# Kernel optimization log

Hardware: AMD Instinct MI355X
Metric: run time of the kernel (lower is better)

## Reference

```python
import jax, jax.numpy as jnp
import numpy as np

N = 8192
D_IN = 512
D_OUT = 64
ALPHA = 0.2  # LeakyReLU negative slope
MASK_VAL = -9e15


def setup_inputs() -> dict:
    key = jax.random.key(0)
    k1, k2, k3, k4 = jax.random.split(key, 4)
    inp = jax.random.normal(k1, (N, D_IN), dtype=jnp.float32)
    adj = (jax.random.uniform(k2, (N, N)) < 0.05).astype(jnp.float32)
    adj = adj.at[jnp.arange(N), jnp.arange(N)].set(1.0)
    W = jax.random.normal(k3, (D_IN, D_OUT), dtype=jnp.float32) * 0.05
    a = jax.random.normal(k4, (2 * D_OUT, 1), dtype=jnp.float32) * 0.05
    return {"input": inp, "adj": adj, "W": W, "a": a}


def reference(input, adj, W, a):
    # h = input @ W : [n, out]
    h = input @ W
    # Algebraic equivalent of the dense pairwise concat:
    # e_ij = leakyrelu([h_i || h_j] . a) = leakyrelu(h_i.a1 + h_j.a2)
    a1, a2 = a[:D_OUT, 0], a[D_OUT:, 0]          # [out], [out]
    e = jax.nn.leaky_relu(
        (h @ a1)[:, None] + (h @ a2)[None, :],    # [n, n]
        negative_slope=ALPHA,
    )
    attention = jnp.where(adj > 0, e, MASK_VAL)
    attention = jax.nn.softmax(attention, axis=1)
    out = attention @ h                            # [n, out]
    return jax.nn.elu(out)                         # end=False branch
```

## Files before the change

### kernel.cpp

```cpp
#include <hip/hip_runtime.h>
#include <hip/hip_bf16.h>

#define N 8192
#define D_IN 512
#define D_OUT 64
#define ALPHA 0.2f
#define BM 16
#define BK 128
#define NSH 32

typedef __attribute__((ext_vector_type(4))) float f32x4;
typedef __attribute__((ext_vector_type(8))) short bf16x8;

static __device__ __forceinline__ unsigned pk_bf16(float lo, float hi) {
    unsigned ulo = __bfloat16_as_ushort(__float2bfloat16(lo));
    unsigned uhi = __bfloat16_as_ushort(__float2bfloat16(hi));
    return (uhi << 16) | ulo;
}

#define BARRIER() do { \
    asm volatile("s_waitcnt lgkmcnt(0)" ::: "memory"); \
    __builtin_amdgcn_sched_barrier(0); \
    __builtin_amdgcn_s_barrier(); \
    __builtin_amdgcn_sched_barrier(0); \
} while (0)

__global__ __launch_bounds__(256) void gat_h_kernel(
    const float* __restrict__ input, const float* __restrict__ W,
    const float* __restrict__ a, unsigned short* __restrict__ hpk,
    float* __restrict__ s1, float* __restrict__ s2)
{
    int wave = (blockIdx.x * 256 + threadIdx.x) >> 6;
    int lane = threadIdx.x & 63;
    int row0 = wave * 4;
    const float* in0 = input + (size_t)row0 * D_IN;
    float a1 = a[lane], a2 = a[D_OUT + lane];
    float acc[4];
#pragma unroll
    for (int r = 0; r < 4; ++r) acc[r] = 0.f;
#pragma unroll 4
    for (int k = 0; k < D_IN; ++k) {
        float wk = W[k * D_OUT + lane];
#pragma unroll
        for (int r = 0; r < 4; ++r)
            acc[r] = fmaf(in0[(size_t)r * D_IN + k], wk, acc[r]);
    }
    {
        int ks = row0 >> 7, kk = (row0 >> 5) & 3, kb = (row0 >> 3) & 3, eo = row0 & 7;
        int wvd = lane >> 4, dd = lane & 15;
        size_t off = ((size_t)(((ks * 4 + wvd) * 4 + kk) * 64) + kb * 16 + dd) * 8 + eo;
        uint2 hv;
        hv.x = pk_bf16(acc[0], acc[1]);
        hv.y = pk_bf16(acc[2], acc[3]);
        *(uint2*)(hpk + off) = hv;
    }
#pragma unroll
    for (int r = 0; r < 4; ++r) {
        float p1 = acc[r] * a1;
        float p2 = acc[r] * a2;
#pragma unroll
        for (int off = 32; off; off >>= 1) {
            p1 += __shfl_xor(p1, off, 64);
            p2 += __shfl_xor(p2, off, 64);
        }
        if (lane == 0) { s1[row0 + r] = p1; s2[row0 + r] = p2; }
    }
}

struct ASP { float4 a0, a1, s0, s1; };
struct UBP { uint4 b0, b1, b2, b3; };

static __device__ __forceinline__ void issue_as(ASP& p, const float* ab,
                                                const float* sb, int j0) {
    p.a0 = *(const float4*)(ab + j0);
    p.a1 = *(const float4*)(ab + j0 + 4);
    p.s0 = *(const float4*)(sb + j0);
    p.s1 = *(const float4*)(sb + j0 + 4);
}
static __device__ __forceinline__ void issue_ub(UBP& p, const unsigned short* hb,
                                                int ksg) {
    const unsigned short* f = hb + ((size_t)ksg << 13);
    p.b0 = *(const uint4*)(f);
    p.b1 = *(const uint4*)(f + 512);
    p.b2 = *(const uint4*)(f + 1024);
    p.b3 = *(const uint4*)(f + 1536);
}

__global__ __launch_bounds__(256, 4) void gat_flash_kernel(
    const float* __restrict__ adj, const unsigned short* __restrict__ hpk,
    const float* __restrict__ s1, const float* __restrict__ s2,
    float* __restrict__ pacc, float* __restrict__ plsum)
{
    __shared__ __align__(16) unsigned char Pl[2][BM * BK * 2];

    const int tid  = threadIdx.x;
    const int lane = tid & 63;
    const int wv   = tid >> 6;
    const int r    = tid >> 4;
    const int s    = tid & 15;
    const int hf   = blockIdx.x >> 9;
    const int rb   = blockIdx.x & 511;
    const int rg   = rb * BM + r;

    const float* adj_base = adj + (size_t)rg * N + hf * 4096 + s * 8;
    const float* s2_base  = s2 + hf * 4096 + s * 8;
    const unsigned short* hb_base = hpk + ((size_t)hf * NSH << 13) + (wv << 11) + (lane << 3);
    float s1r = s1[rg];
    float eref = s1r + s2[rg];
    eref = eref > 0.f ? eref : ALPHA * eref;
    float lsum = 0.f;
    f32x4 acc = {0.f, 0.f, 0.f, 0.f};

    auto stage = [&](const ASP& p, int b) {
        const float* av0 = (const float*)&p.a0;
        const float* av1 = (const float*)&p.a1;
        const float* sv0 = (const float*)&p.s0;
        const float* sv1 = (const float*)&p.s1;
        float w[8];
#pragma unroll
        for (int z = 0; z < 4; ++z) {
            float e0 = s1r + sv0[z]; e0 = e0 > 0.f ? e0 : ALPHA * e0;
            float e1 = s1r + sv1[z]; e1 = e1 > 0.f ? e1 : ALPHA * e1;
            float w0 = __expf(e0 - eref);
            float w1 = __expf(e1 - eref);
            w[z]     = av0[z] > 0.f ? w0 : 0.f;
            w[z + 4] = av1[z] > 0.f ? w1 : 0.f;
        }
#pragma unroll
        for (int z = 0; z < 8; ++z) lsum += w[z];
        uint4 pk;
        pk.x = pk_bf16(w[0], w[1]); pk.y = pk_bf16(w[2], w[3]);
        pk.z = pk_bf16(w[4], w[5]); pk.w = pk_bf16(w[6], w[7]);
        *(uint4*)(&Pl[b][r * 256 + ((s * 16) ^ ((r & 7) << 4))]) = pk;
    };

    auto mfma_step = [&](int c, const UBP& u) {
        const unsigned char* Pc = Pl[c];
        const int i  = lane & 15;
        const int kb = lane >> 4;
        const uint4 ub[4] = {u.b0, u.b1, u.b2, u.b3};
#pragma unroll
        for (int kk = 0; kk < 4; ++kk) {
            uint4 ua = *(const uint4*)(Pc + i * 256 + ((kk * 64 + kb * 16) ^ ((i & 7) << 4)));
            acc = __builtin_amdgcn_mfma_f32_16x16x32_bf16(
                __builtin_bit_cast(bf16x8, ua), __builtin_bit_cast(bf16x8, ub[kk]),
                acc, 0, 0, 0);
        }
    };

    ASP AS_A, AS_B;
    UBP U_A, U_B;
    issue_as(AS_A, adj_base, s2_base, 0);
    issue_as(AS_B, adj_base, s2_base, BK);
    issue_ub(U_A, hb_base, 0);
    issue_ub(U_B, hb_base, 1);
    stage(AS_A, 0);
    issue_as(AS_A, adj_base, s2_base, 2 * BK);
    BARRIER();

    for (int p = 0; p < NSH; p += 2) {
        mfma_step(0, U_A);
        if (p + 2 < NSH) issue_ub(U_A, hb_base, p + 2);
        stage(AS_B, 1);
        if (p + 3 < NSH) issue_as(AS_B, adj_base, s2_base, (p + 3) * BK);
        BARRIER();
        mfma_step(1, U_B);
        if (p + 3 < NSH) issue_ub(U_B, hb_base, p + 3);
        if (p + 2 < NSH) {
            stage(AS_A, 0);
            if (p + 4 < NSH) issue_as(AS_A, adj_base, s2_base, (p + 4) * BK);
        }
        BARRIER();
    }

#pragma unroll
    for (int off = 8; off; off >>= 1) lsum += __shfl_xor(lsum, off, 64);
    if ((tid & 15) == 0) plsum[hf * N + rg] = lsum;

    const int dd = wv * 16 + (lane & 15);
#pragma unroll
    for (int reg = 0; reg < 4; ++reg) {
        int i = (lane >> 4) * 4 + reg;
        pacc[((size_t)hf * N + rb * BM + i) * 64 + dd] = acc[reg];
    }
}

__global__ __launch_bounds__(256) void gat_reduce_kernel(
    const float* __restrict__ pacc, const float* __restrict__ plsum,
    float* __restrict__ out)
{
    int idx = blockIdx.x * 256 + threadIdx.x;
    int row = idx >> 6;
    float aa = pacc[idx] + pacc[(size_t)N * 64 + idx];
    float l  = plsum[row] + plsum[N + row];
    float o  = aa / l;
    out[idx] = o > 0.f ? o : expm1f(o);
}

extern "C" void kernel_launch(void* const* d_in, const int* in_sizes, int n_in,
                              void* d_out, int out_size, void* d_ws, size_t ws_size,
                              hipStream_t stream) {
    const float* input = (const float*)d_in[0];
    const float* adj   = (const float*)d_in[1];
    const float* W     = (const float*)d_in[2];
    const float* a     = (const float*)d_in[3];
    float* out = (float*)d_out;

    unsigned short* hpk = (unsigned short*)d_ws;
    float* s1    = (float*)(hpk + (size_t)N * D_OUT);
    float* s2    = s1 + N;
    float* pacc  = s2 + N;
    float* plsum = pacc + (size_t)2 * N * 64;

    gat_h_kernel<<<512, 256, 0, stream>>>(input, W, a, hpk, s1, s2);
    gat_flash_kernel<<<1024, 256, 0, stream>>>(adj, hpk, s1, s2, pacc, plsum);
    gat_reduce_kernel<<<N * 64 / 256, 256, 0, stream>>>(pacc, plsum, out);
}
```

Before: 114.9 us.

## Feed MFMA A-operand directly from registers and split columns four ways

The attention kernel now computes each lane's bf16 attention weights in exactly the register layout the MFMA A operand expects, so the LDS staging buffer and the per-step barriers go away. Each wave owns its own K slice and computes all four 16-wide output tiles, and the four waves' partial results are reduced through LDS at the end. The column split grows from two to four, giving twice as many blocks, and the reduce kernel is updated to sum four partials. The cost is more partial-output traffic and an extra LDS reduction per block.

```diff
diff --git a/kernel.cpp b/kernel.cpp
--- a/kernel.cpp
+++ b/kernel.cpp
@@ -6,8 +6,9 @@
 #define D_OUT 64
 #define ALPHA 0.2f
 #define BM 16
-#define BK 128
-#define NSH 32
+#define NSPLIT 4
+#define KSEG (N / NSPLIT)
+#define NSH (KSEG / 128)
 
 typedef __attribute__((ext_vector_type(4))) float f32x4;
 typedef __attribute__((ext_vector_type(8))) short bf16x8;
@@ -17,13 +18,6 @@
     unsigned uhi = __bfloat16_as_ushort(__float2bfloat16(hi));
     return (uhi << 16) | ulo;
 }
-
-#define BARRIER() do { \
-    asm volatile("s_waitcnt lgkmcnt(0)" ::: "memory"); \
-    __builtin_amdgcn_sched_barrier(0); \
-    __builtin_amdgcn_s_barrier(); \
-    __builtin_amdgcn_sched_barrier(0); \
-} while (0)
 
 __global__ __launch_bounds__(256) void gat_h_kernel(
     const float* __restrict__ input, const float* __restrict__ W,
@@ -46,9 +40,9 @@
             acc[r] = fmaf(in0[(size_t)r * D_IN + k], wk, acc[r]);
     }
     {
-        int ks = row0 >> 7, kk = (row0 >> 5) & 3, kb = (row0 >> 3) & 3, eo = row0 & 7;
-        int wvd = lane >> 4, dd = lane & 15;
-        size_t off = ((size_t)(((ks * 4 + wvd) * 4 + kk) * 64) + kb * 16 + dd) * 8 + eo;
+        int kw = row0 >> 5, kb = (row0 >> 3) & 3, e0 = row0 & 7;
+        int dw = lane >> 4, dd = lane & 15;
+        size_t off = ((size_t)((kw * 4 + dw) * 64) + kb * 16 + dd) * 8 + e0;
         uint2 hv;
         hv.x = pk_bf16(acc[0], acc[1]);
         hv.y = pk_bf16(acc[2], acc[3]);
@@ -71,15 +65,17 @@
 struct UBP { uint4 b0, b1, b2, b3; };
 
 static __device__ __forceinline__ void issue_as(ASP& p, const float* ab,
-                                                const float* sb, int j0) {
-    p.a0 = *(const float4*)(ab + j0);
-    p.a1 = *(const float4*)(ab + j0 + 4);
-    p.s0 = *(const float4*)(sb + j0);
-    p.s1 = *(const float4*)(sb + j0 + 4);
+                                                const float* sb, int ps) {
+    const float* a = ab + ps * 128;
+    const float* s = sb + ps * 128;
+    p.a0 = *(const float4*)(a);
+    p.a1 = *(const float4*)(a + 4);
+    p.s0 = *(const float4*)(s);
+    p.s1 = *(const float4*)(s + 4);
 }
 static __device__ __forceinline__ void issue_ub(UBP& p, const unsigned short* hb,
-                                                int ksg) {
-    const unsigned short* f = hb + ((size_t)ksg << 13);
+                                                int ps) {
+    const unsigned short* f = hb + ((size_t)ps << 13);
     p.b0 = *(const uint4*)(f);
     p.b1 = *(const uint4*)(f + 512);
     p.b2 = *(const uint4*)(f + 1024);
@@ -91,27 +87,31 @@
     const float* __restrict__ s1, const float* __restrict__ s2,
     float* __restrict__ pacc, float* __restrict__ plsum)
 {
-    __shared__ __align__(16) unsigned char Pl[2][BM * BK * 2];
+    __shared__ float Cl[4][BM][D_OUT];
+    __shared__ float lsl[4][BM];
 
     const int tid  = threadIdx.x;
     const int lane = tid & 63;
-    const int wv   = tid >> 6;
-    const int r    = tid >> 4;
-    const int s    = tid & 15;
+    const int ws   = tid >> 6;
+    const int i    = lane & 15;
+    const int kb   = lane >> 4;
     const int hf   = blockIdx.x >> 9;
     const int rb   = blockIdx.x & 511;
-    const int rg   = rb * BM + r;
-
-    const float* adj_base = adj + (size_t)rg * N + hf * 4096 + s * 8;
-    const float* s2_base  = s2 + hf * 4096 + s * 8;
-    const unsigned short* hb_base = hpk + ((size_t)hf * NSH << 13) + (wv << 11) + (lane << 3);
-    float s1r = s1[rg];
+    const int rg   = rb * BM + i;
+
+    const int col0 = hf * KSEG + ws * 32 + kb * 8;
+    const float* adj_lane = adj + (size_t)rg * N + col0;
+    const float* s2_lane  = s2 + col0;
+    const unsigned short* hb_lane =
+        hpk + (((size_t)(hf * 64 + ws)) << 11) + (lane << 3);
+
+    float s1r  = s1[rg];
     float eref = s1r + s2[rg];
     eref = eref > 0.f ? eref : ALPHA * eref;
     float lsum = 0.f;
-    f32x4 acc = {0.f, 0.f, 0.f, 0.f};
-
-    auto stage = [&](const ASP& p, int b) {
+    f32x4 acc0 = {0,0,0,0}, acc1 = {0,0,0,0}, acc2 = {0,0,0,0}, acc3 = {0,0,0,0};
+
+    auto step = [&](const ASP& p, const UBP& u) {
         const float* av0 = (const float*)&p.a0;
         const float* av1 = (const float*)&p.a1;
         const float* sv0 = (const float*)&p.s0;
@@ -131,58 +131,45 @@
         uint4 pk;
         pk.x = pk_bf16(w[0], w[1]); pk.y = pk_bf16(w[2], w[3]);
         pk.z = pk_bf16(w[4], w[5]); pk.w = pk_bf16(w[6], w[7]);
-        *(uint4*)(&Pl[b][r * 256 + ((s * 16) ^ ((r & 7) << 4))]) = pk;
+        bf16x8 A = __builtin_bit_cast(bf16x8, pk);
+        acc0 = __builtin_amdgcn_mfma_f32_16x16x32_bf16(A, __builtin_bit_cast(bf16x8, u.b0), acc0, 0, 0, 0);
+        acc1 = __builtin_amdgcn_mfma_f32_16x16x32_bf16(A, __builtin_bit_cast(bf16x8, u.b1), acc1, 0, 0, 0);
+        acc2 = __builtin_amdgcn_mfma_f32_16x16x32_bf16(A, __builtin_bit_cast(bf16x8, u.b2), acc2, 0, 0, 0);
+        acc3 = __builtin_amdgcn_mfma_f32_16x16x32_bf16(A, __builtin_bit_cast(bf16x8, u.b3), acc3, 0, 0, 0);
     };
 
-    auto mfma_step = [&](int c, const UBP& u) {
-        const unsigned char* Pc = Pl[c];
-        const int i  = lane & 15;
-        const int kb = lane >> 4;
-        const uint4 ub[4] = {u.b0, u.b1, u.b2, u.b3};
-#pragma unroll
-        for (int kk = 0; kk < 4; ++kk) {
-            uint4 ua = *(const uint4*)(Pc + i * 256 + ((kk * 64 + kb * 16) ^ ((i & 7) << 4)));
-            acc = __builtin_amdgcn_mfma_f32_16x16x32_bf16(
-                __builtin_bit_cast(bf16x8, ua), __builtin_bit_cast(bf16x8, ub[kk]),
-                acc, 0, 0, 0);
-        }
-    };
-
-    ASP AS_A, AS_B;
-    UBP U_A, U_B;
-    issue_as(AS_A, adj_base, s2_base, 0);
-    issue_as(AS_B, adj_base, s2_base, BK);
-    issue_ub(U_A, hb_base, 0);
-    issue_ub(U_B, hb_base, 1);
-    stage(AS_A, 0);
-    issue_as(AS_A, adj_base, s2_base, 2 * BK);
-    BARRIER();
-
+    ASP A0, A1; UBP U0, U1;
+    issue_as(A0, adj_lane, s2_lane, 0); issue_ub(U0, hb_lane, 0);
+    issue_as(A1, adj_lane, s2_lane, 1); issue_ub(U1, hb_lane, 1);
+#pragma unroll 2
     for (int p = 0; p < NSH; p += 2) {
-        mfma_step(0, U_A);
-        if (p + 2 < NSH) issue_ub(U_A, hb_base, p + 2);
-        stage(AS_B, 1);
-        if (p + 3 < NSH) issue_as(AS_B, adj_base, s2_base, (p + 3) * BK);
-        BARRIER();
-        mfma_step(1, U_B);
-        if (p + 3 < NSH) issue_ub(U_B, hb_base, p + 3);
-        if (p + 2 < NSH) {
-            stage(AS_A, 0);
-            if (p + 4 < NSH) issue_as(AS_A, adj_base, s2_base, (p + 4) * BK);
-        }
-        BARRIER();
-    }
-
-#pragma unroll
-    for (int off = 8; off; off >>= 1) lsum += __shfl_xor(lsum, off, 64);
-    if ((tid & 15) == 0) plsum[hf * N + rg] = lsum;
-
-    const int dd = wv * 16 + (lane & 15);
-#pragma unroll
-    for (int reg = 0; reg < 4; ++reg) {
-        int i = (lane >> 4) * 4 + reg;
-        pacc[((size_t)hf * N + rb * BM + i) * 64 + dd] = acc[reg];
-    }
+        step(A0, U0);
+        if (p + 2 < NSH) { issue_as(A0, adj_lane, s2_lane, p + 2); issue_ub(U0, hb_lane, p + 2); }
+        step(A1, U1);
+        if (p + 3 < NSH) { issue_as(A1, adj_lane, s2_lane, p + 3); issue_ub(U1, hb_lane, p + 3); }
+    }
+
+    lsum += __shfl_xor(lsum, 16, 64);
+    lsum += __shfl_xor(lsum, 32, 64);
+    if (lane < 16) lsl[ws][lane] = lsum;
+
+    const f32x4 av[4] = {acc0, acc1, acc2, acc3};
+#pragma unroll
+    for (int dw = 0; dw < 4; ++dw)
+#pragma unroll
+        for (int reg = 0; reg < 4; ++reg)
+            Cl[ws][kb * 4 + reg][dw * 16 + i] = av[dw][reg];
+    __syncthreads();
+
+#pragma unroll
+    for (int o = tid; o < BM * D_OUT; o += 256) {
+        int row = o >> 6, d = o & 63;
+        float v = (Cl[0][row][d] + Cl[1][row][d]) + (Cl[2][row][d] + Cl[3][row][d]);
+        pacc[((size_t)hf * N + rb * BM + row) * 64 + d] = v;
+    }
+    if (tid < BM)
+        plsum[hf * N + rb * BM + tid] =
+            (lsl[0][tid] + lsl[1][tid]) + (lsl[2][tid] + lsl[3][tid]);
 }
 
 __global__ __launch_bounds__(256) void gat_reduce_kernel(
@@ -191,9 +178,13 @@
 {
     int idx = blockIdx.x * 256 + threadIdx.x;
     int row = idx >> 6;
-    float aa = pacc[idx] + pacc[(size_t)N * 64 + idx];
-    float l  = plsum[row] + plsum[N + row];
-    float o  = aa / l;
+    float aa = 0.f, l = 0.f;
+#pragma unroll
+    for (int hf = 0; hf < NSPLIT; ++hf) {
+        aa += pacc[(size_t)hf * N * 64 + idx];
+        l  += plsum[hf * N + row];
+    }
+    float o = aa / l;
     out[idx] = o > 0.f ? o : expm1f(o);
 }
 
@@ -210,9 +201,9 @@
     float* s1    = (float*)(hpk + (size_t)N * D_OUT);
     float* s2    = s1 + N;
     float* pacc  = s2 + N;
-    float* plsum = pacc + (size_t)2 * N * 64;
+    float* plsum = pacc + (size_t)NSPLIT * N * 64;
 
     gat_h_kernel<<<512, 256, 0, stream>>>(input, W, a, hpk, s1, s2);
-    gat_flash_kernel<<<1024, 256, 0, stream>>>(adj, hpk, s1, s2, pacc, plsum);
+    gat_flash_kernel<<<512 * NSPLIT, 256, 0, stream>>>(adj, hpk, s1, s2, pacc, plsum);
     gat_reduce_kernel<<<N * 64 / 256, 256, 0, stream>>>(pacc, plsum, out);
 }
```

Measured after the change: 152.1 us. 1.32x slower.
